# Optimization experiments

Hardware: AMD Instinct MI355X
Metric: run time of the kernel (lower is better)

The kernel has to match this reference:

```python
import jax, jax.numpy as jnp
import numpy as np

T_ENC = 24  # (max_sequence_len + 10) // 3 with max_sequence_len=64
EMB = 1024


def _ln(x, g, b):
    m = jnp.mean(x, -1, keepdims=True)
    v = jnp.var(x, -1, keepdims=True)
    return (x - m) * jax.lax.rsqrt(v + 1e-5) * g + b


def _ts_enc(rc, B, L):
    # recursion_count is a static Python int -> constant encoding vector
    e = np.zeros(T_ENC, np.float32)
    e[0] = rc
    idx = 1 if rc == 1 else 2 if rc == 2 else 3 if rc <= 4 else (rc + 10) // 3 - 1
    e[idx] = 1.0
    return jnp.broadcast_to(jnp.asarray(e), (B, L, T_ENC))


def setup_inputs() -> dict:
    key = jax.random.key(0)
    ks = jax.random.split(key, 12)
    B, L, I, E = 64, 64, 256, EMB
    h1, h2 = 640, 1536  # E-(E-I)//2 and round(1.5*E)
    w = lambda k, s: jax.random.normal(k, s, jnp.float32) * 0.02
    d = {
        "x": jax.random.normal(ks[0], (B, L, I), jnp.float32),
        "se_w1": w(ks[1], (I, h1)), "se_b1": jnp.zeros((h1,), jnp.float32),
        "se_w2": w(ks[2], (h1, E)), "se_b2": jnp.zeros((E,), jnp.float32),
        "enc_w1": w(ks[3], (2 * E + T_ENC, h2)), "enc_b1": jnp.zeros((h2,), jnp.float32),
        "enc_g1": jnp.ones((h2,), jnp.float32), "enc_bb1": jnp.zeros((h2,), jnp.float32),
        "enc_w2": w(ks[4], (h2, E)), "enc_b2": jnp.zeros((E,), jnp.float32),
        "enc_g2": jnp.ones((E,), jnp.float32), "enc_bb2": jnp.zeros((E,), jnp.float32),
        "dec_w1": w(ks[5], (E + T_ENC, h2)), "dec_b1": jnp.zeros((h2,), jnp.float32),
        "dec_g1": jnp.ones((h2,), jnp.float32), "dec_bb1": jnp.zeros((h2,), jnp.float32),
        "dec_w2": w(ks[6], (h2, 2 * E)), "dec_b2": jnp.zeros((2 * E,), jnp.float32),
        "d2_g": jnp.ones((E,), jnp.float32), "d2_b": jnp.zeros((E,), jnp.float32),
        "de_w1": w(ks[7], (E, h1)), "de_b1": jnp.zeros((h1,), jnp.float32),
        "de_w2": w(ks[8], (h1, I)), "de_b2": jnp.zeros((I,), jnp.float32),
    }
    return d


def _forward(x, se_w1, se_b1, se_w2, se_b2,
             enc_w1, enc_b1, enc_g1, enc_bb1, enc_w2, enc_b2, enc_g2, enc_bb2,
             dec_w1, dec_b1, dec_g1, dec_bb1, dec_w2, dec_b2,
             d2_g, d2_b, de_w1, de_b1, de_w2, de_b2):
    B, L, _ = x.shape
    E = EMB
    relu = jax.nn.relu

    # scale_embedding
    x = relu(relu(x @ se_w1 + se_b1) @ se_w2 + se_b2)

    def enc_step(h):
        h = relu(_ln(h @ enc_w1 + enc_b1, enc_g1, enc_bb1))
        return relu(_ln(h @ enc_w2 + enc_b2, enc_g2, enc_bb2))

    def dec_p1(h):
        h = relu(_ln(h @ dec_w1 + dec_b1, dec_g1, dec_bb1))
        return h @ dec_w2 + dec_b2

    def dec_p2(h):
        return relu(_ln(h, d2_g, d2_b))

    # encode: pairwise merge until length 1
    for rc in range(1, L):
        x = jnp.concatenate([x[:, :-1], x[:, 1:]], axis=2)      # [B, Lc, 2E]
        x = jnp.concatenate([x, _ts_enc(rc, B, x.shape[1])], axis=2)
        x = enc_step(x)
    recursion_count = L - 1

    # decode first step: [B,1,E] -> [B,2,E]
    h = jnp.concatenate([x, _ts_enc(recursion_count, B, x.shape[1])], axis=2)
    h = dec_p1(h)
    x = dec_p2(h.reshape(B, 2, E))

    for rc in range(recursion_count - 1, 0, -1):
        h = jnp.concatenate([x, _ts_enc(rc, B, x.shape[1])], axis=2)
        h = dec_p1(h)                                            # [B, Lc, 2E]
        overlap = 0.5 * (h[:, :-1, E:] + h[:, 1:, :E])
        x = jnp.concatenate([h[:, :1, :E], overlap, h[:, -1:, E:]], axis=1)
        x = dec_p2(x)

    # descale_embedding
    return relu(x @ de_w1 + de_b1) @ de_w2 + de_b2


def reference(x, se_w1, se_b1, se_w2, se_b2,
              enc_w1, enc_b1, enc_g1, enc_bb1, enc_w2, enc_b2, enc_g2, enc_bb2,
              dec_w1, dec_b1, dec_g1, dec_bb1, dec_w2, dec_b2,
              d2_g, d2_b, de_w1, de_b1, de_w2, de_b2):
    return _forward(x, se_w1, se_b1, se_w2, se_b2,
                    enc_w1, enc_b1, enc_g1, enc_bb1, enc_w2, enc_b2, enc_g2, enc_bb2,
                    dec_w1, dec_b1, dec_g1, dec_bb1, dec_w2, dec_b2,
                    d2_g, d2_b, de_w1, de_b1, de_w2, de_b2)
```

## Files before the change

### kernel.cpp

```cpp
#include <hip/hip_runtime.h>


typedef _Float16 f16;
typedef _Float16 half8 __attribute__((ext_vector_type(8)));
typedef float floatx4 __attribute__((ext_vector_type(4)));

__device__ __forceinline__ void gld_lds16(const f16* g, f16* l) {
    __builtin_amdgcn_global_load_lds(
        (const __attribute__((address_space(1))) void*)g,
        (__attribute__((address_space(3))) void*)l, 16, 0, 0);
}

template<int MODE, int OUT>
__global__ __launch_bounds__(256, 2) void gemm_s1(
    const f16* __restrict__ Ahi, int lda,
    const f16* __restrict__ Whi,
    const float* __restrict__ bias,
    f16* __restrict__ Chi, float* __restrict__ Cf,
    float* __restrict__ Pf, int ksplit,
    int M, int N, int K, int Kpad, int kbound, int Lo, int Li,
    const f16* __restrict__ tsrow,
    int gy, int q, int r)
{
    __shared__ __align__(16) f16 sm[3][2][128][32];

    const int tid  = threadIdx.x;
    const int lane = tid & 63;
    const int wid  = tid >> 6;

    const int bid = blockIdx.x;
    const int xcd = bid & 7, jj = bid >> 3;
    const int rank = (xcd < r) ? xcd * (q + 1) + jj
                               : r * (q + 1) + (xcd - r) * q + jj;
    const int t  = rank / ksplit;
    const int kz = rank - t * ksplit;
    const int bx = t / gy, by = t - bx * gy;
    const int bm = by * 128;
    const int bn = bx * 128;

    const int rl   = lane >> 2;
    const int kp   = lane & 3;
    const int kofs = ((kp ^ ((rl >> 1) & 3)) << 3);

    const f16* aph[2];
    const f16* wph[2];
    #pragma unroll
    for (int it = 0; it < 2; it++) {
        const int trow = wid * 32 + it * 16 + rl;
        int gr = bm + trow; if (gr > M - 1) gr = M - 1;
        int arow;
        if (MODE == 1) { int b = gr / Lo; int l = gr - b * Lo; arow = b * Li + l; }
        else arow = gr;
        aph[it] = Ahi + (size_t)arow * lda;
        const int col = bn + trow;
        wph[it] = Whi + (size_t)col * K;
    }

    auto stage = [&](int buf, int sstep) {
        const int k0 = sstep << 5;
        #pragma unroll
        for (int it = 0; it < 2; it++) {
            const int lbase = wid * 32 + it * 16;
            const f16* sh;
            if (MODE == 0 || k0 < kbound) sh = aph[it] + (k0 + kofs);
            else                          sh = tsrow + (k0 - kbound) + kofs;
            gld_lds16(sh, &sm[buf][0][lbase][0] + (size_t)lane * 8);
            int kw = k0 + kofs; if (kw > K - 8) kw = K - 8;
            gld_lds16(wph[it] + kw, &sm[buf][1][lbase][0] + (size_t)lane * 8);
        }
    };

    floatx4 acc1[4][4] = {};

    const int nst = Kpad >> 5;
    const int sps = (nst + ksplit - 1) / ksplit;
    const int s0  = kz * sps;
    int s1 = s0 + sps; if (s1 > nst) s1 = nst;

    const int kc  = lane >> 4;
    const int fr  = lane & 15;
    const int wr  = (wid >> 1) * 64;
    const int wc  = (wid & 1) * 64;
    const int ksw = ((kc ^ ((fr >> 1) & 3)) << 3);

    if (s0 < s1) {
        const int n = s1 - s0;
        stage(0, s0);
        stage(1, s0 + ((n > 1) ? 1 : 0));
        for (int j = 0; j < n; j++) {
            asm volatile("s_waitcnt vmcnt(4)" ::: "memory");
            asm volatile("s_barrier" ::: "memory");
            {
                int jt = j + 2; if (jt > n - 1) jt = n - 1;
                stage((j + 2) % 3, s0 + jt);
            }
            const int buf = j % 3;
            half8 ah[4], wh[4];
            #pragma unroll
            for (int m = 0; m < 4; m++)
                ah[m] = *(const half8*)&sm[buf][0][wr + m * 16 + fr][ksw];
            #pragma unroll
            for (int nn = 0; nn < 4; nn++)
                wh[nn] = *(const half8*)&sm[buf][1][wc + nn * 16 + fr][ksw];
            #pragma unroll
            for (int m = 0; m < 4; m++)
                #pragma unroll
                for (int nn = 0; nn < 4; nn++)
                    acc1[m][nn] = __builtin_amdgcn_mfma_f32_16x16x32_f16(ah[m], wh[nn], acc1[m][nn], 0, 0, 0);
        }
        asm volatile("s_waitcnt vmcnt(0)" ::: "memory");
    }

    const int q4 = (lane >> 4) * 4;
    const size_t MN = (size_t)M * N;
    #pragma unroll
    for (int nn = 0; nn < 4; nn++) {
        const int gcol = bn + wc + nn * 16 + fr;
        const float bv = (OUT == 3) ? 0.0f : bias[gcol];
        #pragma unroll
        for (int m = 0; m < 4; m++) {
            #pragma unroll
            for (int j = 0; j < 4; j++) {
                const int grow = bm + wr + m * 16 + q4 + j;
                if (grow < M) {
                    float v = acc1[m][nn][j] + bv;
                    const size_t o = (size_t)grow * N + gcol;
                    if (OUT == 3) {
                        Pf[(size_t)kz * MN + o] = v;
                    } else if (OUT == 2) {
                        Cf[o] = v;
                    } else {
                        Chi[o] = (f16)fmaxf(v, 0.0f);
                    }
                }
            }
        }
    }
}

__global__ void ln_pf(
    const float* __restrict__ P, size_t MN, int ksplit,
    const float* __restrict__ bias, int dual,
    const float* __restrict__ gw, const float* __restrict__ bw,
    f16* __restrict__ oh, int Wd)
{
    const int row = blockIdx.x;
    const size_t base = (size_t)row * Wd;
    const int i8 = threadIdx.x * 8;
    const float* bp = bias + (dual ? ((row & 1) << 10) : 0);

    float v[8];
    {
        const float4 a0 = *(const float4*)(P + base + i8);
        const float4 a1 = *(const float4*)(P + base + i8 + 4);
        v[0]=a0.x; v[1]=a0.y; v[2]=a0.z; v[3]=a0.w;
        v[4]=a1.x; v[5]=a1.y; v[6]=a1.z; v[7]=a1.w;
    }
    for (int z = 1; z < ksplit; z++) {
        const float* Pz = P + (size_t)z * MN + base + i8;
        const float4 c0 = *(const float4*)(Pz);
        const float4 c1 = *(const float4*)(Pz + 4);
        v[0]+=c0.x; v[1]+=c0.y; v[2]+=c0.z; v[3]+=c0.w;
        v[4]+=c1.x; v[5]+=c1.y; v[6]+=c1.z; v[7]+=c1.w;
    }
    float s = 0.f, s2 = 0.f;
    #pragma unroll
    for (int k = 0; k < 8; k++) {
        v[k] += bp[i8 + k];
        s += v[k]; s2 += v[k] * v[k];
    }
    #pragma unroll
    for (int o = 1; o < 64; o <<= 1) { s += __shfl_xor(s, o); s2 += __shfl_xor(s2, o); }
    __shared__ float red[2][4];
    const int nw = blockDim.x >> 6;
    if ((threadIdx.x & 63) == 0) { red[0][threadIdx.x >> 6] = s; red[1][threadIdx.x >> 6] = s2; }
    __syncthreads();
    s = 0.f; s2 = 0.f;
    for (int w = 0; w < nw; w++) { s += red[0][w]; s2 += red[1][w]; }
    const float inv = 1.0f / (float)Wd;
    const float mean = s * inv;
    const float rstd = rsqrtf(s2 * inv - mean * mean + 1e-5f);
    const float4 g0 = *(const float4*)(gw + i8), g1 = *(const float4*)(gw + i8 + 4);
    const float4 b0 = *(const float4*)(bw + i8), b1 = *(const float4*)(bw + i8 + 4);
    const float gg[8] = {g0.x, g0.y, g0.z, g0.w, g1.x, g1.y, g1.z, g1.w};
    const float bb[8] = {b0.x, b0.y, b0.z, b0.w, b1.x, b1.y, b1.z, b1.w};
    half8 ho;
    #pragma unroll
    for (int k = 0; k < 8; k++)
        ho[k] = (f16)fmaxf((v[k] - mean) * rstd * gg[k] + bb[k], 0.0f);
    *(half8*)(oh + base + i8) = ho;
}

__global__ void comb_pf(
    const float* __restrict__ P, size_t MN, int ksplit,
    const float* __restrict__ bias,
    const float* __restrict__ gw, const float* __restrict__ bw,
    f16* __restrict__ oh, int Liv)
{
    const int row = blockIdx.x;
    const int Lp = Liv + 1;
    const int b = row / Lp, j = row - b * Lp;
    const int i8 = threadIdx.x * 8;

    auto sum8 = [&](size_t off, float* acc) {
        const float4 a0 = *(const float4*)(P + off);
        const float4 a1 = *(const float4*)(P + off + 4);
        acc[0]=a0.x; acc[1]=a0.y; acc[2]=a0.z; acc[3]=a0.w;
        acc[4]=a1.x; acc[5]=a1.y; acc[6]=a1.z; acc[7]=a1.w;
        for (int z = 1; z < ksplit; z++) {
            const float* Pz = P + (size_t)z * MN + off;
            const float4 c0 = *(const float4*)(Pz);
            const float4 c1 = *(const float4*)(Pz + 4);
            acc[0]+=c0.x; acc[1]+=c0.y; acc[2]+=c0.z; acc[3]+=c0.w;
            acc[4]+=c1.x; acc[5]+=c1.y; acc[6]+=c1.z; acc[7]+=c1.w;
        }
    };

    float v[8];
    if (j == 0) {
        sum8((size_t)(b * Liv) * 2048 + i8, v);
        #pragma unroll
        for (int k = 0; k < 8; k++) v[k] += bias[i8 + k];
    } else if (j == Liv) {
        sum8((size_t)(b * Liv + Liv - 1) * 2048 + 1024 + i8, v);
        #pragma unroll
        for (int k = 0; k < 8; k++) v[k] += bias[1024 + i8 + k];
    } else {
        float u[8];
        sum8((size_t)(b * Liv + j - 1) * 2048 + 1024 + i8, v);
        sum8((size_t)(b * Liv + j) * 2048 + i8, u);
        #pragma unroll
        for (int k = 0; k < 8; k++)
            v[k] = 0.5f * ((v[k] + bias[1024 + i8 + k]) + (u[k] + bias[i8 + k]));
    }
    float s = 0.f, s2 = 0.f;
    #pragma unroll
    for (int k = 0; k < 8; k++) { s += v[k]; s2 += v[k] * v[k]; }
    #pragma unroll
    for (int o = 1; o < 64; o <<= 1) { s += __shfl_xor(s, o); s2 += __shfl_xor(s2, o); }
    __shared__ float red[2][2];
    if ((threadIdx.x & 63) == 0) { red[0][threadIdx.x >> 6] = s; red[1][threadIdx.x >> 6] = s2; }
    __syncthreads();
    s = red[0][0] + red[0][1]; s2 = red[1][0] + red[1][1];
    const float mean = s * 9.765625e-4f;
    const float rstd = rsqrtf(s2 * 9.765625e-4f - mean * mean + 1e-5f);
    const float4 g0 = *(const float4*)(gw + i8), g1 = *(const float4*)(gw + i8 + 4);
    const float4 b0 = *(const float4*)(bw + i8), b1 = *(const float4*)(bw + i8 + 4);
    const float gg[8] = {g0.x, g0.y, g0.z, g0.w, g1.x, g1.y, g1.z, g1.w};
    const float bb[8] = {b0.x, b0.y, b0.z, b0.w, b1.x, b1.y, b1.z, b1.w};
    const size_t ob = (size_t)row * 1024 + i8;
    half8 ho;
    #pragma unroll
    for (int k = 0; k < 8; k++)
        ho[k] = (f16)fmaxf((v[k] - mean) * rstd * gg[k] + bb[k], 0.0f);
    *(half8*)(oh + ob) = ho;
}

__global__ __launch_bounds__(256) void wt_f16_k(
    const float* __restrict__ W, f16* __restrict__ Th, int K, int N)
{
    __shared__ float t[64][65];
    const int k0 = blockIdx.x * 64, n0 = blockIdx.y * 64;
    {
        const int j = threadIdx.x & 63, i0 = (threadIdx.x >> 6) * 16;
        for (int ii = 0; ii < 16; ii++) {
            int k = k0 + i0 + ii;
            t[i0 + ii][j] = (k < K) ? W[(size_t)k * N + n0 + j] : 0.f;
        }
    }
    __syncthreads();
    const int i = threadIdx.x & 63, j0 = (threadIdx.x >> 6) * 16;
    const int k = k0 + i;
    if (k < K) {
        for (int jj = 0; jj < 16; jj++)
            Th[(size_t)(n0 + j0 + jj) * K + k] = (f16)t[i][j0 + jj];
    }
}

__global__ void split_x_v(const float* __restrict__ x, f16* __restrict__ h, int n8) {
    int i = blockIdx.x * 256 + threadIdx.x;
    if (i >= n8) return;
    const int i8 = i * 8;
    const float4 f0 = *(const float4*)(x + i8), f1 = *(const float4*)(x + i8 + 4);
    const float vv[8] = {f0.x, f0.y, f0.z, f0.w, f1.x, f1.y, f1.z, f1.w};
    half8 ho;
    #pragma unroll
    for (int k = 0; k < 8; k++) ho[k] = (f16)vv[k];
    *(half8*)(h + i8) = ho;
}

__global__ void ts_init_k(f16* __restrict__ ts) {
    int e = blockIdx.x * 256 + threadIdx.x;
    if (e < 2048) {
        int rc = e >> 5, c = e & 31;
        float v = 0.f;
        if (rc >= 1) {
            int idx = (rc == 1) ? 1 : (rc == 2) ? 2 : (rc <= 4) ? 3 : ((rc + 10) / 3 - 1);
            if (c == 0) v = (float)rc;
            else if (c == idx) v = 1.f;
        }
        ts[e] = (f16)v;
    }
}

extern "C" void kernel_launch(void* const* d_in, const int* in_sizes, int n_in,
                              void* d_out, int out_size, void* d_ws, size_t ws_size,
                              hipStream_t stream)
{
    const float* xin    = (const float*)d_in[0];
    const float* se_w1  = (const float*)d_in[1];
    const float* se_b1  = (const float*)d_in[2];
    const float* se_w2  = (const float*)d_in[3];
    const float* se_b2  = (const float*)d_in[4];
    const float* enc_w1 = (const float*)d_in[5];
    const float* enc_b1 = (const float*)d_in[6];
    const float* enc_g1 = (const float*)d_in[7];
    const float* enc_bb1= (const float*)d_in[8];
    const float* enc_w2 = (const float*)d_in[9];
    const float* enc_b2 = (const float*)d_in[10];
    const float* enc_g2 = (const float*)d_in[11];
    const float* enc_bb2= (const float*)d_in[12];
    const float* dec_w1 = (const float*)d_in[13];
    const float* dec_b1 = (const float*)d_in[14];
    const float* dec_g1 = (const float*)d_in[15];
    const float* dec_bb1= (const float*)d_in[16];
    const float* dec_w2 = (const float*)d_in[17];
    const float* dec_b2 = (const float*)d_in[18];
    const float* d2_g   = (const float*)d_in[19];
    const float* d2_b   = (const float*)d_in[20];
    const float* de_w1  = (const float*)d_in[21];
    const float* de_b1  = (const float*)d_in[22];
    const float* de_w2  = (const float*)d_in[23];
    const float* de_b2  = (const float*)d_in[24];

    const size_t ws_f16 = ws_size / 2;
    f16* ws = (f16*)d_ws;
    f16* Xh = ws;
    f16* Hh = Xh + 4194304;
    f16* WR = ws + (ws_f16 - 4757504);
    f16* TS = WR + 4755456;
    float* PF = (float*)(Hh + 6193152);
    const long long pcap_ll = ((long long)ws_f16 - 4757504ll - 4194304ll - 6193152ll) / 2;
    const size_t pcap = (pcap_ll > 0) ? (size_t)pcap_ll : 0;
    const bool dec_unchunk = pcap >= 8257536ull;

    ts_init_k<<<8, 256, 0, stream>>>(TS);

    auto wt = [&](const float* W, int K, int N, f16* Th) {
        wt_f16_k<<<dim3((K + 63) / 64, N / 64), 256, 0, stream>>>(W, Th, K, N);
    };
    auto pick_ks = [&](int natural, int nst, size_t MN) {
        int ks = (natural >= 448) ? 1 : (448 + natural - 1) / natural;
        if (ks > 8) ks = 8;
        if (ks > nst) ks = nst;
        while (ks > 1 && (size_t)ks * MN > pcap) ks--;
        return ks;
    };

    #define GEMM(MODE, OUT, Ah, lda, Wh, bias, Ch, Cf, Pfp, ks, M, N, K, Kpad, kb, Lo, Li, tsr) \
        do { \
            const int gx_ = (N) / 128, gy_ = ((M) + 127) / 128;                \
            const int nwg_ = gx_ * gy_ * (ks);                                 \
            gemm_s1<MODE, OUT><<<nwg_, 256, 0, stream>>>(                      \
                Ah, lda, Wh, bias, Ch, Cf, Pfp, (ks),                          \
                M, N, K, Kpad, kb, Lo, Li, tsr, gy_, nwg_ >> 3, nwg_ & 7);     \
        } while (0)

    {
        f16* W1h = WR;            f16* W2h = W1h + 163840;
        wt(se_w1, 256, 640, W1h);
        wt(se_w2, 640, 1024, W2h);
        f16* Sh  = (f16*)PF;
        f16* H1h = Sh + 1048576;
        split_x_v<<<512, 256, 0, stream>>>(xin, Sh, 131072);
        GEMM(0, 1, Sh, 256, W1h, se_b1, H1h, (float*)0, (float*)0, 1,
             4096, 640, 256, 256, 256, 0, 0, TS);
        GEMM(0, 1, H1h, 640, W2h, se_b2, Xh, (float*)0, (float*)0, 1,
             4096, 1024, 640, 640, 640, 0, 0, TS);
    }

    {
        f16* E1h = WR;             f16* E2h = E1h + 3182592;
        wt(enc_w1, 2072, 1536, E1h);
        wt(enc_w2, 1536, 1024, E2h);
        for (int rc = 1; rc <= 63; rc++) {
            const int Lo = 64 - rc, Li = Lo + 1, Mc = 64 * Lo;
            const int gy = (Mc + 127) / 128;
            const int k1 = pick_ks(12 * gy, 65, (size_t)Mc * 1536);
            GEMM(1, 3, Xh, 1024, E1h, enc_b1, (f16*)0, (float*)0,
                 PF, k1, Mc, 1536, 2072, 2080, 2048, Lo, Li, TS + rc * 32);
            ln_pf<<<Mc, 192, 0, stream>>>(PF, (size_t)Mc * 1536, k1, enc_b1, 0,
                                          enc_g1, enc_bb1, Hh, 1536);
            const int k2 = pick_ks(8 * gy, 48, (size_t)Mc * 1024);
            GEMM(0, 3, Hh, 1536, E2h, enc_b2, (f16*)0, (float*)0,
                 PF, k2, Mc, 1024, 1536, 1536, 1536, 0, 0, TS);
            ln_pf<<<Mc, 128, 0, stream>>>(PF, (size_t)Mc * 1024, k2, enc_b2, 0,
                                          enc_g2, enc_bb2, Xh, 1024);
        }
    }

    {
        f16* D1h = WR;             f16* D2h = D1h + 1609728;
        wt(dec_w1, 1048, 1536, D1h);
        wt(dec_w2, 1536, 2048, D2h);

        {
            const int k1 = pick_ks(12, 33, (size_t)64 * 1536);
            GEMM(2, 3, Xh, 1024, D1h, dec_b1, (f16*)0, (float*)0,
                 PF, k1, 64, 1536, 1048, 1056, 1024, 0, 0, TS + 63 * 32);
            ln_pf<<<64, 192, 0, stream>>>(PF, (size_t)64 * 1536, k1, dec_b1, 0,
                                          dec_g1, dec_bb1, Hh, 1536);
            const int k2 = pick_ks(16, 48, (size_t)64 * 2048);
            GEMM(0, 3, Hh, 1536, D2h, dec_b2, (f16*)0, (float*)0,
                 PF, k2, 64, 2048, 1536, 1536, 1536, 0, 0, TS);
            ln_pf<<<128, 128, 0, stream>>>(PF, (size_t)64 * 2048, k2, dec_b2, 1,
                                           d2_g, d2_b, Xh, 1024);
        }

        for (int rc = 62; rc >= 1; rc--) {
            const int Li = 64 - rc;
            const int nch = (!dec_unchunk && 64 * Li > 2016) ? 2 : 1, nb = 64 / nch;
            for (int c = nch - 1; c >= 0; c--) {
                const int b0 = c * nb, Mc = nb * Li;
                const size_t ai = (size_t)b0 * Li * 1024;
                const size_t oi = (size_t)b0 * (Li + 1) * 1024;
                const int gy = (Mc + 127) / 128;
                const int k1 = pick_ks(12 * gy, 33, (size_t)Mc * 1536);
                GEMM(2, 3, Xh + ai, 1024, D1h, dec_b1, (f16*)0, (float*)0,
                     PF, k1, Mc, 1536, 1048, 1056, 1024, 0, 0, TS + rc * 32);
                ln_pf<<<Mc, 192, 0, stream>>>(PF, (size_t)Mc * 1536, k1, dec_b1, 0,
                                              dec_g1, dec_bb1, Hh, 1536);
                const int k2 = pick_ks(16 * gy, 48, (size_t)Mc * 2048);
                GEMM(0, 3, Hh, 1536, D2h, dec_b2, (f16*)0, (float*)0,
                     PF, k2, Mc, 2048, 1536, 1536, 1536, 0, 0, TS);
                comb_pf<<<nb * (Li + 1), 128, 0, stream>>>(
                    PF, (size_t)Mc * 2048, k2, dec_b2, d2_g, d2_b,
                    Xh + oi, Li);
            }
        }
    }

    {
        f16* W1h = WR;            f16* W2h = W1h + 655360;
        wt(de_w1, 1024, 640, W1h);
        wt(de_w2, 640, 256, W2h);
        f16* H1h = (f16*)PF;
        GEMM(0, 1, Xh, 1024, W1h, de_b1, H1h, (float*)0, (float*)0, 1,
             4096, 640, 1024, 1024, 1024, 0, 0, TS);
        GEMM(0, 2, H1h, 640, W2h, de_b2, (f16*)0, (float*)d_out, (float*)0, 1,
             4096, 256, 640, 640, 640, 0, 0, TS);
    }
    #undef GEMM
}
```

Baseline: 7.848 ms.

## Add 128x256 wide-tile GEMM variant for N divisible by 256

```diff
diff --git a/kernel.cpp b/kernel.cpp
--- a/kernel.cpp
+++ b/kernel.cpp
@@ -24,9 +24,8 @@
 {
     __shared__ __align__(16) f16 sm[3][2][128][32];
 
-    const int tid  = threadIdx.x;
-    const int lane = tid & 63;
-    const int wid  = tid >> 6;
+    const int lane = threadIdx.x & 63;
+    const int wid  = threadIdx.x >> 6;
 
     const int bid = blockIdx.x;
     const int xcd = bid & 7, jj = bid >> 3;
@@ -125,13 +124,137 @@
                 if (grow < M) {
                     float v = acc1[m][nn][j] + bv;
                     const size_t o = (size_t)grow * N + gcol;
-                    if (OUT == 3) {
-                        Pf[(size_t)kz * MN + o] = v;
-                    } else if (OUT == 2) {
-                        Cf[o] = v;
-                    } else {
-                        Chi[o] = (f16)fmaxf(v, 0.0f);
-                    }
+                    if (OUT == 3)      Pf[(size_t)kz * MN + o] = v;
+                    else if (OUT == 2) Cf[o] = v;
+                    else               Chi[o] = (f16)fmaxf(v, 0.0f);
+                }
+            }
+        }
+    }
+}
+
+template<int MODE, int OUT>
+__global__ __launch_bounds__(256, 2) void gemm_w2(
+    const f16* __restrict__ Ahi, int lda,
+    const f16* __restrict__ Whi,
+    const float* __restrict__ bias,
+    f16* __restrict__ Chi, float* __restrict__ Cf,
+    float* __restrict__ Pf, int ksplit,
+    int M, int N, int K, int Kpad, int kbound, int Lo, int Li,
+    const f16* __restrict__ tsrow,
+    int gy, int q, int r)
+{
+    __shared__ __align__(16) f16 smA[3][128][32];
+    __shared__ __align__(16) f16 smW[3][256][32];
+
+    const int lane = threadIdx.x & 63;
+    const int wid  = threadIdx.x >> 6;
+
+    const int bid = blockIdx.x;
+    const int xcd = bid & 7, jj = bid >> 3;
+    const int rank = (xcd < r) ? xcd * (q + 1) + jj
+                               : r * (q + 1) + (xcd - r) * q + jj;
+    const int t  = rank / ksplit;
+    const int kz = rank - t * ksplit;
+    const int bx = t / gy, by = t - bx * gy;
+    const int bm = by * 128;
+    const int bn = bx * 256;
+
+    const int rl   = lane >> 2;
+    const int kp   = lane & 3;
+    const int kofs = ((kp ^ ((rl >> 1) & 3)) << 3);
+
+    const f16* aph[2];
+    const f16* wph[4];
+    #pragma unroll
+    for (int it = 0; it < 2; it++) {
+        const int trow = wid * 32 + it * 16 + rl;
+        int gr = bm + trow; if (gr > M - 1) gr = M - 1;
+        int arow;
+        if (MODE == 1) { int b = gr / Lo; int l = gr - b * Lo; arow = b * Li + l; }
+        else arow = gr;
+        aph[it] = Ahi + (size_t)arow * lda;
+    }
+    #pragma unroll
+    for (int it = 0; it < 4; it++) {
+        const int col = bn + wid * 64 + it * 16 + rl;
+        wph[it] = Whi + (size_t)col * K;
+    }
+
+    auto stage = [&](int buf, int sstep) {
+        const int k0 = sstep << 5;
+        #pragma unroll
+        for (int it = 0; it < 2; it++) {
+            const f16* sh;
+            if (MODE == 0 || k0 < kbound) sh = aph[it] + (k0 + kofs);
+            else                          sh = tsrow + (k0 - kbound) + kofs;
+            gld_lds16(sh, &smA[buf][wid * 32 + it * 16][0] + (size_t)lane * 8);
+        }
+        #pragma unroll
+        for (int it = 0; it < 4; it++) {
+            int kw = k0 + kofs; if (kw > K - 8) kw = K - 8;
+            gld_lds16(wph[it] + kw, &smW[buf][wid * 64 + it * 16][0] + (size_t)lane * 8);
+        }
+    };
+
+    floatx4 acc1[4][8] = {};
+
+    const int nst = Kpad >> 5;
+    const int sps = (nst + ksplit - 1) / ksplit;
+    const int s0  = kz * sps;
+    int s1 = s0 + sps; if (s1 > nst) s1 = nst;
+
+    const int kc  = lane >> 4;
+    const int fr  = lane & 15;
+    const int wr  = (wid >> 1) * 64;
+    const int wc  = (wid & 1) * 128;
+    const int ksw = ((kc ^ ((fr >> 1) & 3)) << 3);
+
+    if (s0 < s1) {
+        const int n = s1 - s0;
+        stage(0, s0);
+        stage(1, s0 + ((n > 1) ? 1 : 0));
+        for (int j = 0; j < n; j++) {
+            asm volatile("s_waitcnt vmcnt(6)" ::: "memory");
+            asm volatile("s_barrier" ::: "memory");
+            {
+                int jt = j + 2; if (jt > n - 1) jt = n - 1;
+                stage((j + 2) % 3, s0 + jt);
+            }
+            const int buf = j % 3;
+            half8 ah[4], wh[8];
+            #pragma unroll
+            for (int m = 0; m < 4; m++)
+                ah[m] = *(const half8*)&smA[buf][wr + m * 16 + fr][ksw];
+            #pragma unroll
+            for (int nn = 0; nn < 8; nn++)
+                wh[nn] = *(const half8*)&smW[buf][wc + nn * 16 + fr][ksw];
+            #pragma unroll
+            for (int m = 0; m < 4; m++)
+                #pragma unroll
+                for (int nn = 0; nn < 8; nn++)
+                    acc1[m][nn] = __builtin_amdgcn_mfma_f32_16x16x32_f16(ah[m], wh[nn], acc1[m][nn], 0, 0, 0);
+        }
+        asm volatile("s_waitcnt vmcnt(0)" ::: "memory");
+    }
+
+    const int q4 = (lane >> 4) * 4;
+    const size_t MN = (size_t)M * N;
+    #pragma unroll
+    for (int nn = 0; nn < 8; nn++) {
+        const int gcol = bn + wc + nn * 16 + fr;
+        const float bv = (OUT == 3) ? 0.0f : bias[gcol];
+        #pragma unroll
+        for (int m = 0; m < 4; m++) {
+            #pragma unroll
+            for (int j = 0; j < 4; j++) {
+                const int grow = bm + wr + m * 16 + q4 + j;
+                if (grow < M) {
+                    float v = acc1[m][nn][j] + bv;
+                    const size_t o = (size_t)grow * N + gcol;
+                    if (OUT == 3)      Pf[(size_t)kz * MN + o] = v;
+                    else if (OUT == 2) Cf[o] = v;
+                    else               Chi[o] = (f16)fmaxf(v, 0.0f);
                 }
             }
         }
@@ -349,8 +472,11 @@
     auto wt = [&](const float* W, int K, int N, f16* Th) {
         wt_f16_k<<<dim3((K + 63) / 64, N / 64), 256, 0, stream>>>(W, Th, K, N);
     };
-    auto pick_ks = [&](int natural, int nst, size_t MN) {
-        int ks = (natural >= 448) ? 1 : (448 + natural - 1) / natural;
+    auto pick_ks = [&](int M, int N, int nst, size_t MN) {
+        const int gx = ((N & 255) == 0) ? (N / 256) : (N / 128);
+        const int gy = (M + 127) / 128;
+        const int nat = gx * gy;
+        int ks = (nat >= 448) ? 1 : (448 + nat - 1) / nat;
         if (ks > 8) ks = 8;
         if (ks > nst) ks = nst;
         while (ks > 1 && (size_t)ks * MN > pcap) ks--;
@@ -359,11 +485,18 @@
 
     #define GEMM(MODE, OUT, Ah, lda, Wh, bias, Ch, Cf, Pfp, ks, M, N, K, Kpad, kb, Lo, Li, tsr) \
         do { \
-            const int gx_ = (N) / 128, gy_ = ((M) + 127) / 128;                \
-            const int nwg_ = gx_ * gy_ * (ks);                                 \
-            gemm_s1<MODE, OUT><<<nwg_, 256, 0, stream>>>(                      \
-                Ah, lda, Wh, bias, Ch, Cf, Pfp, (ks),                          \
-                M, N, K, Kpad, kb, Lo, Li, tsr, gy_, nwg_ >> 3, nwg_ & 7);     \
+            const int gy_ = ((M) + 127) / 128;                                     \
+            if (((N) & 255) == 0) {                                                \
+                const int nwg_ = ((N) / 256) * gy_ * (ks);                         \
+                gemm_w2<MODE, OUT><<<nwg_, 256, 0, stream>>>(                      \
+                    Ah, lda, Wh, bias, Ch, Cf, Pfp, (ks),                          \
+                    M, N, K, Kpad, kb, Lo, Li, tsr, gy_, nwg_ >> 3, nwg_ & 7);     \
+            } else {                                                               \
+                const int nwg_ = ((N) / 128) * gy_ * (ks);                         \
+                gemm_s1<MODE, OUT><<<nwg_, 256, 0, stream>>>(                      \
+                    Ah, lda, Wh, bias, Ch, Cf, Pfp, (ks),                          \
+                    M, N, K, Kpad, kb, Lo, Li, tsr, gy_, nwg_ >> 3, nwg_ & 7);     \
+            }                                                                      \
         } while (0)
 
     {
@@ -385,13 +518,12 @@
         wt(enc_w2, 1536, 1024, E2h);
         for (int rc = 1; rc <= 63; rc++) {
             const int Lo = 64 - rc, Li = Lo + 1, Mc = 64 * Lo;
-            const int gy = (Mc + 127) / 128;
-            const int k1 = pick_ks(12 * gy, 65, (size_t)Mc * 1536);
+            const int k1 = pick_ks(Mc, 1536, 65, (size_t)Mc * 1536);
             GEMM(1, 3, Xh, 1024, E1h, enc_b1, (f16*)0, (float*)0,
                  PF, k1, Mc, 1536, 2072, 2080, 2048, Lo, Li, TS + rc * 32);
             ln_pf<<<Mc, 192, 0, stream>>>(PF, (size_t)Mc * 1536, k1, enc_b1, 0,
                                           enc_g1, enc_bb1, Hh, 1536);
-            const int k2 = pick_ks(8 * gy, 48, (size_t)Mc * 1024);
+            const int k2 = pick_ks(Mc, 1024, 48, (size_t)Mc * 1024);
             GEMM(0, 3, Hh, 1536, E2h, enc_b2, (f16*)0, (float*)0,
                  PF, k2, Mc, 1024, 1536, 1536, 1536, 0, 0, TS);
             ln_pf<<<Mc, 128, 0, stream>>>(PF, (size_t)Mc * 1024, k2, enc_b2, 0,
@@ -405,12 +537,12 @@
         wt(dec_w2, 1536, 2048, D2h);
 
         {
-            const int k1 = pick_ks(12, 33, (size_t)64 * 1536);
+            const int k1 = pick_ks(64, 1536, 33, (size_t)64 * 1536);
             GEMM(2, 3, Xh, 1024, D1h, dec_b1, (f16*)0, (float*)0,
                  PF, k1, 64, 1536, 1048, 1056, 1024, 0, 0, TS + 63 * 32);
             ln_pf<<<64, 192, 0, stream>>>(PF, (size_t)64 * 1536, k1, dec_b1, 0,
                                           dec_g1, dec_bb1, Hh, 1536);
-            const int k2 = pick_ks(16, 48, (size_t)64 * 2048);
+            const int k2 = pick_ks(64, 2048, 48, (size_t)64 * 2048);
             GEMM(0, 3, Hh, 1536, D2h, dec_b2, (f16*)0, (float*)0,
                  PF, k2, 64, 2048, 1536, 1536, 1536, 0, 0, TS);
             ln_pf<<<128, 128, 0, stream>>>(PF, (size_t)64 * 2048, k2, dec_b2, 1,
@@ -424,13 +556,12 @@
                 const int b0 = c * nb, Mc = nb * Li;
                 const size_t ai = (size_t)b0 * Li * 1024;
                 const size_t oi = (size_t)b0 * (Li + 1) * 1024;
-                const int gy = (Mc + 127) / 128;
-                const int k1 = pick_ks(12 * gy, 33, (size_t)Mc * 1536);
+                const int k1 = pick_ks(Mc, 1536, 33, (size_t)Mc * 1536);
                 GEMM(2, 3, Xh + ai, 1024, D1h, dec_b1, (f16*)0, (float*)0,
                      PF, k1, Mc, 1536, 1048, 1056, 1024, 0, 0, TS + rc * 32);
                 ln_pf<<<Mc, 192, 0, stream>>>(PF, (size_t)Mc * 1536, k1, dec_b1, 0,
                                               dec_g1, dec_bb1, Hh, 1536);
-                const int k2 = pick_ks(16 * gy, 48, (size_t)Mc * 2048);
+                const int k2 = pick_ks(Mc, 2048, 48, (size_t)Mc * 2048);
                 GEMM(0, 3, Hh, 1536, D2h, dec_b2, (f16*)0, (float*)0,
                      PF, k2, Mc, 2048, 1536, 1536, 1536, 0, 0, TS);
                 comb_pf<<<nb * (Li + 1), 128, 0, stream>>>(
```

Result: slower. 10.33 ms (+31.6%).
